# Kernel tuning notes

Hardware: AMD Instinct MI355X
Metric: run time of the kernel (lower is better)

## Reference

```python
import jax, jax.numpy as jnp
import numpy as np

H = 1024      # hidden_size
NH = 16       # num_heads
HD = H // NH  # head_dim
E = 4096      # expand_size
EPS = 1e-5


def layernorm(x, w, b):
    mu = jnp.mean(x, axis=-1, keepdims=True)
    var = jnp.mean(jnp.square(x - mu), axis=-1, keepdims=True)
    return (x - mu) * jax.lax.rsqrt(var + EPS) * w + b


def setup_inputs() -> dict:
    key = jax.random.key(0)
    ks = jax.random.split(key, 8)
    s = 1.0 / np.sqrt(H)
    return {
        "x": jax.random.normal(ks[0], (4, 2048, H), dtype=jnp.float32),
        "ln1_w": jnp.ones((H,), jnp.float32),
        "ln1_b": jnp.zeros((H,), jnp.float32),
        "Wqkv": jax.random.normal(ks[1], (H, 3 * H), dtype=jnp.float32) * s,
        "bqkv": jnp.zeros((3 * H,), jnp.float32),
        "Wo": jax.random.normal(ks[2], (H, H), dtype=jnp.float32) * s,
        "bo": jnp.zeros((H,), jnp.float32),
        "ln2_w": jnp.ones((H,), jnp.float32),
        "ln2_b": jnp.zeros((H,), jnp.float32),
        "fc1_w": jax.random.normal(ks[3], (H, E), dtype=jnp.float32) * s,
        "fc1_b": jnp.zeros((E,), jnp.float32),
        "fc2_w": jax.random.normal(ks[4], (E, H), dtype=jnp.float32) * (1.0 / np.sqrt(E)),
        "fc2_b": jnp.zeros((H,), jnp.float32),
    }


def reference(x, ln1_w, ln1_b, Wqkv, bqkv, Wo, bo, ln2_w, ln2_b, fc1_w, fc1_b, fc2_w, fc2_b):
    B, S, C = x.shape
    # --- attention sub-block (pre-norm) ---
    h = layernorm(x, ln1_w, ln1_b)
    qkv = h @ Wqkv + bqkv                             # [B,S,3C]
    qkv = qkv.reshape(B, S, 3, NH, HD)
    q, k, v = (jnp.moveaxis(qkv[:, :, i], 2, 1) for i in range(3))  # [B,NH,S,HD]
    attn = jnp.einsum("bhqd,bhkd->bhqk", q, k) / np.sqrt(HD)        # [B,NH,S,S]
    attn = jax.nn.softmax(attn, axis=-1)
    o = jnp.einsum("bhqk,bhkd->bhqd", attn, v)        # [B,NH,S,HD]
    o = jnp.moveaxis(o, 1, 2).reshape(B, S, C)
    x = x + o @ Wo + bo
    # --- FFN sub-block (pre-norm) ---
    h = layernorm(x, ln2_w, ln2_b)
    h = jax.nn.gelu(h @ fc1_w + fc1_b, approximate=False)
    return x + h @ fc2_w + fc2_b
```

## Files before the change

kernel.cpp:

```cpp
#include <hip/hip_runtime.h>
#include <hip/hip_bf16.h>
#include <math.h>

typedef __bf16 bf16_t;
typedef __bf16 bf16x4 __attribute__((ext_vector_type(4)));
typedef short  s16x8  __attribute__((ext_vector_type(8)));
typedef float  f32x4  __attribute__((ext_vector_type(4)));

#define DEVINL __device__ __forceinline__

DEVINL void gload_lds16(const void* g, void* l) {
  __builtin_amdgcn_global_load_lds(
      (const __attribute__((address_space(1))) unsigned int*)g,
      (__attribute__((address_space(3))) unsigned int*)l, 16, 0, 0);
}

DEVINL f32x4 mfma16(s16x8 a, s16x8 b, f32x4 c) {
  return __builtin_amdgcn_mfma_f32_16x16x32_bf16(a, b, c, 0, 0, 0);
}

DEVINL float fexp2(float x) { return __builtin_amdgcn_exp2f(x); }

__global__ __launch_bounds__(256) void tcast_kernel(const float* __restrict__ W,
                                                    bf16_t* __restrict__ WT,
                                                    int K, int N) {
  __shared__ float tile[32][33];
  const int n0 = blockIdx.x * 32, k0 = blockIdx.y * 32;
  const int tx = threadIdx.x, ty = threadIdx.y;
#pragma unroll
  for (int j = 0; j < 4; ++j)
    tile[ty + j * 8][tx] = W[(size_t)(k0 + ty + j * 8) * N + (n0 + tx)];
  __syncthreads();
#pragma unroll
  for (int j = 0; j < 4; ++j)
    WT[(size_t)(n0 + ty + j * 8) * K + (k0 + tx)] = (bf16_t)tile[tx][ty + j * 8];
}

__global__ __launch_bounds__(256) void ln_kernel(const float* __restrict__ x,
                                                 const float* __restrict__ w,
                                                 const float* __restrict__ b,
                                                 bf16_t* __restrict__ out) {
  const int row = blockIdx.x, tid = threadIdx.x;
  const float4 v = ((const float4*)(x + (size_t)row * 1024))[tid];
  float s  = v.x + v.y + v.z + v.w;
  float s2 = v.x * v.x + v.y * v.y + v.z * v.z + v.w * v.w;
#pragma unroll
  for (int off = 32; off > 0; off >>= 1) {
    s  += __shfl_down(s, off);
    s2 += __shfl_down(s2, off);
  }
  __shared__ float red[8];
  const int wave = tid >> 6, lane = tid & 63;
  if (lane == 0) { red[wave] = s; red[4 + wave] = s2; }
  __syncthreads();
  s  = red[0] + red[1] + red[2] + red[3];
  s2 = red[4] + red[5] + red[6] + red[7];
  const float mu = s * (1.0f / 1024.0f);
  const float rs = rsqrtf(s2 * (1.0f / 1024.0f) - mu * mu + 1e-5f);
  const float4 wv = ((const float4*)w)[tid];
  const float4 bv = ((const float4*)b)[tid];
  bf16x4 o;
  o[0] = (bf16_t)((v.x - mu) * rs * wv.x + bv.x);
  o[1] = (bf16_t)((v.y - mu) * rs * wv.y + bv.y);
  o[2] = (bf16_t)((v.z - mu) * rs * wv.z + bv.z);
  o[3] = (bf16_t)((v.w - mu) * rs * wv.w + bv.w);
  ((bf16x4*)(out + (size_t)row * 1024))[tid] = o;
}

template <int EPI>
__global__ __launch_bounds__(256, 4) void gemm128b(const bf16_t* __restrict__ A,
                                                   const bf16_t* __restrict__ BT,
                                                   const float* __restrict__ bias,
                                                   const float* __restrict__ resid,
                                                   void* __restrict__ out,
                                                   void* __restrict__ out2,
                                                   int M, int N, int K) {
  __shared__ __align__(16) bf16_t sA[128 * 64];
  __shared__ __align__(16) bf16_t sB[128 * 64];
  const int tid = threadIdx.x;
  const int lane = tid & 63, wave = tid >> 6;
  const int wr = wave >> 1, wc = wave & 1;
  const int g = lane >> 4, lr = lane & 15;

  const int bid = blockIdx.x;
  const int cpx = gridDim.x >> 3;
  const int gid = (bid & 7) * cpx + (bid >> 3);
  const int m0 = (gid & 63) * 128, n0 = (gid >> 6) * 128;
  const bf16_t* Ab = A + (size_t)m0 * K;
  const bf16_t* Bb = BT + (size_t)n0 * K;

  f32x4 acc[4][4] = {};

  for (int kt = 0; kt < K; kt += 64) {
    __syncthreads();
#pragma unroll
    for (int q = 0; q < 4; ++q) {
      const int c = q * 256 + tid;
      const int r = c >> 3;
      const int j = (c & 7) ^ (r & 7);
      const size_t doff = (size_t)(q * 256 + wave * 64) * 8;
      gload_lds16(Ab + (size_t)r * K + kt + j * 8, sA + doff);
      gload_lds16(Bb + (size_t)r * K + kt + j * 8, sB + doff);
    }
    __syncthreads();
#pragma unroll
    for (int ks = 0; ks < 2; ++ks) {
      s16x8 af[4], bfr[4];
#pragma unroll
      for (int m = 0; m < 4; ++m) {
        const int r = wr * 64 + m * 16 + lr;
        af[m] = *(const s16x8*)&sA[r * 64 + (((ks << 2) + g) ^ (r & 7)) * 8];
      }
#pragma unroll
      for (int n = 0; n < 4; ++n) {
        const int r = wc * 64 + n * 16 + lr;
        bfr[n] = *(const s16x8*)&sB[r * 64 + (((ks << 2) + g) ^ (r & 7)) * 8];
      }
#pragma unroll
      for (int m = 0; m < 4; ++m)
#pragma unroll
        for (int n = 0; n < 4; ++n)
          acc[m][n] = mfma16(af[m], bfr[n], acc[m][n]);
    }
  }

#pragma unroll
  for (int m = 0; m < 4; ++m)
#pragma unroll
    for (int n = 0; n < 4; ++n) {
      const int col = n0 + wc * 64 + n * 16 + lr;
      const float bv = bias[col];
      const int rrow0 = m0 + wr * 64 + m * 16 + g * 4;
      if (EPI == 3 && col >= 2048) {
        const int col2 = col - 2048;
        bf16x4 pk;
#pragma unroll
        for (int i = 0; i < 4; ++i) pk[i] = (bf16_t)(acc[m][n][i] + bv);
        const size_t didx =
            ((((size_t)(rrow0 >> 11)) * 16 + (col2 >> 6)) * 64 + (col2 & 63)) * 2048 +
            (rrow0 & 2047);
        *(bf16x4*)&((bf16_t*)out2)[didx] = pk;
      } else {
#pragma unroll
        for (int i = 0; i < 4; ++i) {
          const int rrow = rrow0 + i;
          float v = acc[m][n][i] + bv;
          if (EPI == 1) {
            const size_t idx = (size_t)rrow * N + col;
            v += resid[idx];
            ((float*)out)[idx] = v;
          } else if (EPI == 2) {
            v = 0.5f * v * (1.0f + erff(v * 0.70710678118f));
            ((bf16_t*)out)[(size_t)rrow * N + col] = (bf16_t)v;
          } else if (EPI == 3) {
            ((bf16_t*)out)[(size_t)rrow * 2048 + col] = (bf16_t)v;
          } else {
            ((bf16_t*)out)[(size_t)rrow * N + col] = (bf16_t)v;
          }
        }
      }
    }
}

__global__ __launch_bounds__(256) void flash_attn7(const bf16_t* __restrict__ qk,
                                                   const bf16_t* __restrict__ vt,
                                                   bf16_t* __restrict__ O) {
  const int S = 2048;
  const int bid = blockIdx.x;
  const int swz = (bid & 7) * 256 + (bid >> 3);
  const int bh = swz >> 5;
  const int qt = swz & 31;
  const int h = bh & 15;
  const size_t rowbase = (size_t)(bh >> 4) * S;
  const int tid = threadIdx.x, lane = tid & 63, wave = tid >> 6;
  const int g = lane >> 4, lr = lane & 15;
  const int q0w = qt * 64 + wave * 16;
  const float c2 = 0.18033688f;

  __shared__ __align__(16) bf16_t sK[64 * 64];
  __shared__ __align__(16) bf16_t sVT[64 * 64];
  __shared__ __align__(16) bf16_t sP[4][16 * 72];

  const bf16_t* vtb = vt + (size_t)bh * 64 * 2048;

  s16x8 aq[2];
  {
    const bf16_t* qrow = qk + (rowbase + q0w + lr) * 2048 + h * 64;
    aq[0] = *(const s16x8*)(qrow + g * 8);
    aq[1] = *(const s16x8*)(qrow + 32 + g * 8);
  }

  f32x4 oa[4] = {};
  float m2 = -1e30f, lrun = 0.0f;

  for (int kv0 = 0; kv0 < S; kv0 += 64) {
    __syncthreads();
#pragma unroll
    for (int p = 0; p < 2; ++p) {
      const int c = p * 256 + wave * 64 + lane;
      const int r = c >> 3;
      const int pb = (c & 7) ^ (r & 7);
      char* dK = (char*)sK + (size_t)(p * 256 + wave * 64) * 16;
      char* dV = (char*)sVT + (size_t)(p * 256 + wave * 64) * 16;
      gload_lds16(qk + (rowbase + kv0 + r) * 2048 + 1024 + h * 64 + pb * 8, dK);
      gload_lds16(vtb + (size_t)r * 2048 + kv0 + pb * 8, dV);
    }
    __syncthreads();

    f32x4 sc[4] = {};
#pragma unroll
    for (int st = 0; st < 2; ++st)
#pragma unroll
      for (int fr = 0; fr < 4; ++fr) {
        const int pb = (g + 4 * st) ^ (lr & 7);
        const s16x8 ak = *(const s16x8*)&sK[(fr * 16 + lr) * 64 + pb * 8];
        sc[fr] = mfma16(ak, aq[st], sc[fr]);
      }

    float rmax = fmaxf(fmaxf(sc[0][0], sc[0][1]), fmaxf(sc[0][2], sc[0][3]));
#pragma unroll
    for (int fr = 1; fr < 4; ++fr)
#pragma unroll
      for (int i = 0; i < 4; ++i) rmax = fmaxf(rmax, sc[fr][i]);
    rmax = fmaxf(rmax, __shfl_xor(rmax, 16));
    rmax = fmaxf(rmax, __shfl_xor(rmax, 32));
    const float pm2 = rmax * c2;
    if (!__all(pm2 <= m2 + 8.0f)) {
      const float mn = fmaxf(m2, pm2);
      const float alpha = fexp2(m2 - mn);
      m2 = mn;
      lrun *= alpha;
#pragma unroll
      for (int f2 = 0; f2 < 4; ++f2)
#pragma unroll
        for (int i = 0; i < 4; ++i) oa[f2][i] *= alpha;
    }
    float rsum = 0.0f;
#pragma unroll
    for (int fr = 0; fr < 4; ++fr)
#pragma unroll
      for (int i = 0; i < 4; ++i) {
        const float pp = fexp2(fmaf(sc[fr][i], c2, -m2));
        sc[fr][i] = pp;
        rsum += pp;
      }
    rsum += __shfl_xor(rsum, 16);
    rsum += __shfl_xor(rsum, 32);
    lrun += rsum;

#pragma unroll
    for (int fr = 0; fr < 4; ++fr) {
      bf16x4 pk;
#pragma unroll
      for (int i = 0; i < 4; ++i) pk[i] = (bf16_t)sc[fr][i];
      *(bf16x4*)&sP[wave][lr * 72 + fr * 16 + 4 * g] = pk;
    }

#pragma unroll
    for (int st = 0; st < 2; ++st) {
      const s16x8 pa = *(const s16x8*)&sP[wave][lr * 72 + st * 32 + g * 8];
#pragma unroll
      for (int f2 = 0; f2 < 4; ++f2) {
        const int pb = (g + 4 * st) ^ (lr & 7);
        const s16x8 va = *(const s16x8*)&sVT[(f2 * 16 + lr) * 64 + pb * 8];
        oa[f2] = mfma16(va, pa, oa[f2]);
      }
    }
  }

  const float rl = 1.0f / lrun;
#pragma unroll
  for (int f2 = 0; f2 < 4; ++f2) {
    bf16x4 ov;
#pragma unroll
    for (int i = 0; i < 4; ++i) ov[i] = (bf16_t)(oa[f2][i] * rl);
    *(bf16x4*)&O[(rowbase + q0w + lr) * 1024 + h * 64 + f2 * 16 + 4 * g] = ov;
  }
}

extern "C" void kernel_launch(void* const* d_in, const int* in_sizes, int n_in,
                              void* d_out, int out_size, void* d_ws, size_t ws_size,
                              hipStream_t stream) {
  const float* x    = (const float*)d_in[0];
  const float* ln1w = (const float*)d_in[1];
  const float* ln1b = (const float*)d_in[2];
  const float* Wqkv = (const float*)d_in[3];
  const float* bqkv = (const float*)d_in[4];
  const float* Wo   = (const float*)d_in[5];
  const float* bo   = (const float*)d_in[6];
  const float* ln2w = (const float*)d_in[7];
  const float* ln2b = (const float*)d_in[8];
  const float* fc1w = (const float*)d_in[9];
  const float* fc1b = (const float*)d_in[10];
  const float* fc2w = (const float*)d_in[11];
  const float* fc2b = (const float*)d_in[12];

  const int M = 8192;

  char* ws = (char*)d_ws;
  size_t off = 0;
  auto alloc = [&](size_t bytes) {
    char* p = ws + off;
    off += (bytes + 255) & ~(size_t)255;
    return p;
  };
  bf16_t* WqkvT = (bf16_t*)alloc((size_t)3072 * 1024 * 2);
  bf16_t* WoT   = (bf16_t*)alloc((size_t)1024 * 1024 * 2);
  bf16_t* fc1T  = (bf16_t*)alloc((size_t)4096 * 1024 * 2);
  bf16_t* fc2T  = (bf16_t*)alloc((size_t)1024 * 4096 * 2);
  bf16_t* h1    = (bf16_t*)alloc((size_t)M * 1024 * 2);
  bf16_t* qkQK  = (bf16_t*)alloc((size_t)M * 2048 * 2);
  bf16_t* vTg   = (bf16_t*)alloc((size_t)M * 1024 * 2);
  bf16_t* attnO = (bf16_t*)alloc((size_t)M * 1024 * 2);
  float*  x2    = (float*)alloc((size_t)M * 1024 * 4);
  bf16_t* h2   = h1;
  bf16_t* gbuf = qkQK;
  if (off > ws_size) return;

  const dim3 tb(32, 8);
  tcast_kernel<<<dim3(96, 32), tb, 0, stream>>>(Wqkv, WqkvT, 1024, 3072);
  tcast_kernel<<<dim3(32, 32), tb, 0, stream>>>(Wo, WoT, 1024, 1024);
  tcast_kernel<<<dim3(128, 32), tb, 0, stream>>>(fc1w, fc1T, 1024, 4096);
  tcast_kernel<<<dim3(32, 128), tb, 0, stream>>>(fc2w, fc2T, 4096, 1024);

  ln_kernel<<<M, 256, 0, stream>>>(x, ln1w, ln1b, h1);

  gemm128b<3><<<dim3(1536), 256, 0, stream>>>(h1, WqkvT, bqkv, nullptr, qkQK, vTg, M, 3072, 1024);

  flash_attn7<<<dim3(2048), 256, 0, stream>>>(qkQK, vTg, attnO);

  gemm128b<1><<<dim3(512), 256, 0, stream>>>(attnO, WoT, bo, x, x2, nullptr, M, 1024, 1024);

  ln_kernel<<<M, 256, 0, stream>>>(x2, ln2w, ln2b, h2);

  gemm128b<2><<<dim3(2048), 256, 0, stream>>>(h2, fc1T, fc1b, nullptr, gbuf, nullptr, M, 4096, 1024);

  gemm128b<1><<<dim3(512), 256, 0, stream>>>(gbuf, fc2T, fc2b, x2, (float*)d_out, nullptr, M, 1024, 4096);
}
```

Before: 438.4 us.

## Switch flash attention to 32x32 MFMA with 128-query tiles per block

The attention kernel now uses 32x32x16 bf16 MFMA instead of 16x16x32. Each wave handles 32 query rows instead of 16, so a block covers 128 queries and the grid is halved. The aim is to amortize the K/V tile loads into LDS over twice as many queries and to issue fewer, larger MFMA instructions. In exchange, register pressure rises because of the 16-wide accumulators, and there are fewer blocks to spread across CUs.

Result: no change. 433.3 us (-1.2%).

```diff
diff --git a/kernel.cpp b/kernel.cpp
--- a/kernel.cpp
+++ b/kernel.cpp
@@ -6,6 +6,7 @@
 typedef __bf16 bf16x4 __attribute__((ext_vector_type(4)));
 typedef short  s16x8  __attribute__((ext_vector_type(8)));
 typedef float  f32x4  __attribute__((ext_vector_type(4)));
+typedef float  f32x16 __attribute__((ext_vector_type(16)));
 
 #define DEVINL __device__ __forceinline__
 
@@ -17,6 +18,10 @@
 
 DEVINL f32x4 mfma16(s16x8 a, s16x8 b, f32x4 c) {
   return __builtin_amdgcn_mfma_f32_16x16x32_bf16(a, b, c, 0, 0, 0);
+}
+
+DEVINL f32x16 mfma32(s16x8 a, s16x8 b, f32x16 c) {
+  return __builtin_amdgcn_mfma_f32_32x32x16_bf16(a, b, c, 0, 0, 0);
 }
 
 DEVINL float fexp2(float x) { return __builtin_amdgcn_exp2f(x); }
@@ -162,35 +167,36 @@
     }
 }
 
-__global__ __launch_bounds__(256) void flash_attn7(const bf16_t* __restrict__ qk,
+__global__ __launch_bounds__(256) void flash_attn8(const bf16_t* __restrict__ qk,
                                                    const bf16_t* __restrict__ vt,
                                                    bf16_t* __restrict__ O) {
   const int S = 2048;
   const int bid = blockIdx.x;
-  const int swz = (bid & 7) * 256 + (bid >> 3);
-  const int bh = swz >> 5;
-  const int qt = swz & 31;
+  const int swz = (bid & 7) * 128 + (bid >> 3);
+  const int bh = swz >> 4;
+  const int qt = swz & 15;
   const int h = bh & 15;
   const size_t rowbase = (size_t)(bh >> 4) * S;
   const int tid = threadIdx.x, lane = tid & 63, wave = tid >> 6;
-  const int g = lane >> 4, lr = lane & 15;
-  const int q0w = qt * 64 + wave * 16;
+  const int ql = lane & 31;
+  const int H = lane >> 5;
+  const int q0w = qt * 128 + wave * 32;
   const float c2 = 0.18033688f;
 
   __shared__ __align__(16) bf16_t sK[64 * 64];
   __shared__ __align__(16) bf16_t sVT[64 * 64];
-  __shared__ __align__(16) bf16_t sP[4][16 * 72];
+  __shared__ __align__(16) bf16_t sP[4][32 * 64];
 
   const bf16_t* vtb = vt + (size_t)bh * 64 * 2048;
 
-  s16x8 aq[2];
+  s16x8 qf[4];
   {
-    const bf16_t* qrow = qk + (rowbase + q0w + lr) * 2048 + h * 64;
-    aq[0] = *(const s16x8*)(qrow + g * 8);
-    aq[1] = *(const s16x8*)(qrow + 32 + g * 8);
+    const bf16_t* qrow = qk + (rowbase + q0w + ql) * 2048 + h * 64 + 8 * H;
+#pragma unroll
+    for (int ks = 0; ks < 4; ++ks) qf[ks] = *(const s16x8*)(qrow + 16 * ks);
   }
 
-  f32x4 oa[4] = {};
+  f32x16 oa[2] = {};
   float m2 = -1e30f, lrun = 0.0f;
 
   for (int kv0 = 0; kv0 < S; kv0 += 64) {
@@ -207,22 +213,21 @@
     }
     __syncthreads();
 
-    f32x4 sc[4] = {};
-#pragma unroll
-    for (int st = 0; st < 2; ++st)
-#pragma unroll
-      for (int fr = 0; fr < 4; ++fr) {
-        const int pb = (g + 4 * st) ^ (lr & 7);
-        const s16x8 ak = *(const s16x8*)&sK[(fr * 16 + lr) * 64 + pb * 8];
-        sc[fr] = mfma16(ak, aq[st], sc[fr]);
-      }
-
-    float rmax = fmaxf(fmaxf(sc[0][0], sc[0][1]), fmaxf(sc[0][2], sc[0][3]));
-#pragma unroll
-    for (int fr = 1; fr < 4; ++fr)
-#pragma unroll
-      for (int i = 0; i < 4; ++i) rmax = fmaxf(rmax, sc[fr][i]);
-    rmax = fmaxf(rmax, __shfl_xor(rmax, 16));
+    f32x16 sc[2] = {};
+#pragma unroll
+    for (int ks = 0; ks < 4; ++ks)
+#pragma unroll
+      for (int kvf = 0; kvf < 2; ++kvf) {
+        const int R = kvf * 32 + ql;
+        const s16x8 ak = *(const s16x8*)&sK[R * 64 + (((2 * ks + H) ^ (R & 7)) * 8)];
+        sc[kvf] = mfma32(ak, qf[ks], sc[kvf]);
+      }
+
+    float rmax = sc[0][0];
+#pragma unroll
+    for (int f = 0; f < 2; ++f)
+#pragma unroll
+      for (int r = 0; r < 16; ++r) rmax = fmaxf(rmax, sc[f][r]);
     rmax = fmaxf(rmax, __shfl_xor(rmax, 32));
     const float pm2 = rmax * c2;
     if (!__all(pm2 <= m2 + 8.0f)) {
@@ -231,51 +236,57 @@
       m2 = mn;
       lrun *= alpha;
 #pragma unroll
-      for (int f2 = 0; f2 < 4; ++f2)
-#pragma unroll
-        for (int i = 0; i < 4; ++i) oa[f2][i] *= alpha;
+      for (int f = 0; f < 2; ++f)
+#pragma unroll
+        for (int r = 0; r < 16; ++r) oa[f][r] *= alpha;
     }
     float rsum = 0.0f;
 #pragma unroll
-    for (int fr = 0; fr < 4; ++fr)
-#pragma unroll
-      for (int i = 0; i < 4; ++i) {
-        const float pp = fexp2(fmaf(sc[fr][i], c2, -m2));
-        sc[fr][i] = pp;
+    for (int f = 0; f < 2; ++f)
+#pragma unroll
+      for (int r = 0; r < 16; ++r) {
+        const float pp = fexp2(fmaf(sc[f][r], c2, -m2));
+        sc[f][r] = pp;
         rsum += pp;
       }
-    rsum += __shfl_xor(rsum, 16);
     rsum += __shfl_xor(rsum, 32);
     lrun += rsum;
 
 #pragma unroll
-    for (int fr = 0; fr < 4; ++fr) {
-      bf16x4 pk;
-#pragma unroll
-      for (int i = 0; i < 4; ++i) pk[i] = (bf16_t)sc[fr][i];
-      *(bf16x4*)&sP[wave][lr * 72 + fr * 16 + 4 * g] = pk;
-    }
-
-#pragma unroll
-    for (int st = 0; st < 2; ++st) {
-      const s16x8 pa = *(const s16x8*)&sP[wave][lr * 72 + st * 32 + g * 8];
-#pragma unroll
-      for (int f2 = 0; f2 < 4; ++f2) {
-        const int pb = (g + 4 * st) ^ (lr & 7);
-        const s16x8 va = *(const s16x8*)&sVT[(f2 * 16 + lr) * 64 + pb * 8];
-        oa[f2] = mfma16(va, pa, oa[f2]);
+    for (int ks = 0; ks < 4; ++ks)
+#pragma unroll
+      for (int hi = 0; hi < 2; ++hi) {
+        const int f = ks >> 1, rb = 8 * (ks & 1) + 4 * hi;
+        bf16x4 pk;
+#pragma unroll
+        for (int e = 0; e < 4; ++e) pk[e] = (bf16_t)sc[f][rb + e];
+        const int slot = ((2 * ks + hi) + ql) & 7;
+        *(bf16x4*)&sP[wave][ql * 64 + slot * 8 + 4 * H] = pk;
+      }
+
+#pragma unroll
+    for (int ks = 0; ks < 4; ++ks) {
+      const s16x8 pbf = *(const s16x8*)&sP[wave][ql * 64 + (((2 * ks + H) + ql) & 7) * 8];
+#pragma unroll
+      for (int df = 0; df < 2; ++df) {
+        const int R = df * 32 + ql;
+        const s16x8 va = *(const s16x8*)&sVT[R * 64 + (((2 * ks + H) ^ (R & 7)) * 8)];
+        oa[df] = mfma32(va, pbf, oa[df]);
       }
     }
   }
 
   const float rl = 1.0f / lrun;
 #pragma unroll
-  for (int f2 = 0; f2 < 4; ++f2) {
-    bf16x4 ov;
-#pragma unroll
-    for (int i = 0; i < 4; ++i) ov[i] = (bf16_t)(oa[f2][i] * rl);
-    *(bf16x4*)&O[(rowbase + q0w + lr) * 1024 + h * 64 + f2 * 16 + 4 * g] = ov;
-  }
+  for (int df = 0; df < 2; ++df)
+#pragma unroll
+    for (int rr = 0; rr < 4; ++rr) {
+      bf16x4 ov;
+#pragma unroll
+      for (int e = 0; e < 4; ++e) ov[e] = (bf16_t)(oa[df][4 * rr + e] * rl);
+      const int d0 = 32 * df + 8 * rr + 4 * H;
+      *(bf16x4*)&O[(rowbase + q0w + ql) * 1024 + h * 64 + d0] = ov;
+    }
 }
 
 extern "C" void kernel_launch(void* const* d_in, const int* in_sizes, int n_in,
@@ -327,7 +338,7 @@
 
   gemm128b<3><<<dim3(1536), 256, 0, stream>>>(h1, WqkvT, bqkv, nullptr, qkQK, vTg, M, 3072, 1024);
 
-  flash_attn7<<<dim3(2048), 256, 0, stream>>>(qkQK, vTg, attnO);
+  flash_attn8<<<dim3(1024), 256, 0, stream>>>(qkQK, vTg, attnO);
 
   gemm128b<1><<<dim3(512), 256, 0, stream>>>(attnO, WoT, bo, x, x2, nullptr, M, 1024, 1024);
 
```
